# Kernel optimization log

Measured on AMD Instinct MI355X. Metric: run time of the kernel, lower is better.

## Reference

```python
import jax, jax.numpy as jnp
import numpy as np
from jax import lax

B, H, W, DIM = 64, 32, 32, 448
HEADS, DH, WS = 8, 28, 8
INNER = DH * HEADS            # 224
C2 = DIM // 2                 # 224 (spatial branch channels == inner_dim)
HALF = INNER // 2             # 112 per attention sub-branch
SEQ_L1 = WS * WS              # 64 tokens per window
SEQ_L2 = (256 // HEADS) ** 2 // SEQ_L1  # 16 == number of windows (32x32 map)
SCALE = DH ** -0.5


def setup_inputs() -> dict:
    key = jax.random.key(0)
    ks = jax.random.split(key, 18)
    def nrm(k, shape, s):
        return jax.random.normal(k, shape, jnp.float32) * s
    inp = {}
    inp["x"] = jax.random.normal(ks[0], (B, H, W, DIM), jnp.float32)
    # trunc_normal_(std=1) positional biases -> clipped normals
    inp["pos_emb1"] = jnp.clip(jax.random.normal(ks[1], (1, 1, HEADS // 2, SEQ_L1, SEQ_L1), jnp.float32), -2.0, 2.0)
    inp["pos_emb2"] = jnp.clip(jax.random.normal(ks[2], (1, 1, HEADS // 2, SEQ_L2, SEQ_L2), jnp.float32), -2.0, 2.0)
    # linear weights stored (in, out)
    inp["Wq"] = nrm(ks[3], (C2, INNER), 0.02)
    inp["Wkv"] = nrm(ks[4], (C2, 2 * INNER), 0.02)
    inp["Wout"] = nrm(ks[5], (INNER, DIM), 0.02)
    inp["bout"] = nrm(ks[6], (DIM,), 0.02)
    # 3D conv weights (O, I, D, Kh, Kw), fan-in = 224*27 -> std ~ 0.01
    for i, name in enumerate(["convr", "conv1", "conv2", "conv3"]):
        inp[name + "_w"] = nrm(ks[7 + 2 * i], (C2, C2, 3, 3, 3), 0.01)
        inp[name + "_b"] = nrm(ks[8 + 2 * i], (C2,), 0.01)
    return inp


def _conv3d(t, w, b):
    y = lax.conv_general_dilated(t, w, (1, 1, 1), [(1, 1)] * 3,
                                 dimension_numbers=("NCDHW", "OIDHW", "NCDHW"))
    return y + b[None, :, None, None, None]


def _window(t):
    # [b, H, W, c] -> [b, n_windows, ws*ws, c]
    b, h, w, c = t.shape
    t = t.reshape(b, h // WS, WS, w // WS, WS, c).transpose(0, 1, 3, 2, 4, 5)
    return t.reshape(b, (h // WS) * (w // WS), WS * WS, c)


def _unwindow(t):
    # [b, n_windows, ws*ws, c] -> [b, H, W, c]
    b, n, m, c = t.shape
    t = t.reshape(b, H // WS, W // WS, WS, WS, c).transpose(0, 1, 3, 2, 4, 5)
    return t.reshape(b, H, W, c)


def _split_heads(t):
    # [b, n, m, half] -> [b, n, heads//2, m, dh]
    b, n, m, c = t.shape
    return t.reshape(b, n, m, HEADS // 2, DH).transpose(0, 1, 3, 2, 4)


def _merge_heads(t):
    # [b, n, heads//2, m, dh] -> [b, n, m, half]
    b, n, h, m, d = t.shape
    return t.transpose(0, 1, 3, 2, 4).reshape(b, n, m, h * d)


def _attn(q, q_, k, v, pos):
    del q_
    sim = jnp.einsum("bnhid,bnhjd->bnhij", q * SCALE, k) + pos
    a = jax.nn.softmax(sim, axis=-1)
    return jnp.einsum("bnhij,bnhjd->bnhid", a, v)


def reference(x, pos_emb1, pos_emb2, Wq, Wkv, Wout, bout,
              convr_w, convr_b, conv1_w, conv1_b, conv2_w, conv2_b, conv3_w, conv3_b):
    b = x.shape[0]
    x1 = x[..., :C2]
    x2 = x[..., C2:]
    # spectral 3D conv branch: [b, c2, 1, H, W]
    x2 = x2.transpose(0, 3, 1, 2)[:, :, None]
    res = jax.nn.relu(_conv3d(x2, convr_w, convr_b))
    o = jax.nn.relu(_conv3d(x2, conv1_w, conv1_b))
    o = jax.nn.relu(_conv3d(o, conv2_w, conv2_b))
    o = jax.nn.relu(_conv3d(o, conv3_w, conv3_b))
    X2S = (o + res)[:, :, 0].transpose(0, 2, 3, 1)  # [b, H, W, c2]

    q = x1 @ Wq
    kv = x1 @ Wkv
    k, v = kv[..., :INNER], kv[..., INNER:]
    q1, q2 = q[..., :HALF], q[..., HALF:]
    k1, k2 = k[..., :HALF], k[..., HALF:]
    v1, v2 = v[..., :HALF], v[..., HALF:]

    # local (within-window) branch
    q1h, k1h, v1h = map(lambda t: _split_heads(_window(t)), (q1, k1, v1))
    sim1 = jnp.einsum("bnhid,bnhjd->bnhij", q1h * SCALE, k1h) + pos_emb1
    out1 = jnp.einsum("bnhij,bnhjd->bnhid", jax.nn.softmax(sim1, axis=-1), v1h)
    out1 = _merge_heads(out1)  # [b, n, m, half]

    # grid (across-window) branch: swap window/token axes
    q2h, k2h, v2h = map(lambda t: _split_heads(_window(t).transpose(0, 2, 1, 3)), (q2, k2, v2))
    sim2 = jnp.einsum("bnhid,bnhjd->bnhij", q2h * SCALE, k2h) + pos_emb2
    out2 = jnp.einsum("bnhij,bnhjd->bnhid", jax.nn.softmax(sim2, axis=-1), v2h)
    out2 = _merge_heads(out2).transpose(0, 2, 1, 3)  # [b, n, m, half]

    out = jnp.concatenate([out1, out2], axis=-1) @ Wout + bout  # [b, n, m, DIM]
    out = _unwindow(out)
    return jnp.concatenate([out, X2S], axis=-1)  # [b, H, W, DIM + C2]
```

## Files before the change

### kernel.cpp

```cpp
#include <hip/hip_runtime.h>

typedef unsigned short u16;
typedef unsigned int   u32;
typedef __attribute__((ext_vector_type(4))) float  f32x4;
typedef __attribute__((ext_vector_type(8))) short  s16x8;
typedef __attribute__((ext_vector_type(8))) __bf16 bf16x8;
typedef __attribute__((ext_vector_type(2))) u32    u32x2;

#define DEV __device__ __forceinline__
#define SCALE_Q 0.1889822365046136f

DEV float bf2f(u16 u){ u32 x = ((u32)u)<<16; float f; __builtin_memcpy(&f,&x,4); return f; }
DEV u16   f2bf(float f){ u32 x; __builtin_memcpy(&x,&f,4); return (u16)((x + 0x7fffu + ((x>>16)&1u))>>16); }

DEV s16x8 cvt8(const float* __restrict__ src){
  f32x4 f0 = *(const f32x4*)src, f1 = *(const f32x4*)(src+4);
  bf16x8 b;
  b[0]=(__bf16)f0[0]; b[1]=(__bf16)f0[1]; b[2]=(__bf16)f0[2]; b[3]=(__bf16)f0[3];
  b[4]=(__bf16)f1[0]; b[5]=(__bf16)f1[1]; b[6]=(__bf16)f1[2]; b[7]=(__bf16)f1[3];
  return __builtin_bit_cast(s16x8, b);
}

DEV void gll16(const u16* g, u16* l){
  __builtin_amdgcn_global_load_lds(
      (const __attribute__((address_space(1))) u32*)(const void*)g,
      (__attribute__((address_space(3))) u32*)(void*)l,
      16, 0, 0);
}

DEV void ld28(const u16* __restrict__ p, float* dst, float scale){
#pragma unroll
  for (int j=0;j<7;j++){
    u32x2 w = *(const u32x2*)(p + j*4);
    dst[j*4+0] = bf2f((u16)(w[0]&0xffffu))*scale;
    dst[j*4+1] = bf2f((u16)(w[0]>>16))*scale;
    dst[j*4+2] = bf2f((u16)(w[1]&0xffffu))*scale;
    dst[j*4+3] = bf2f((u16)(w[1]>>16))*scale;
  }
}

__global__ void pack_k(const float* __restrict__ Wq, const float* __restrict__ Wkv,
                       const float* __restrict__ Wout,
                       const float* __restrict__ wr, const float* __restrict__ w1,
                       const float* __restrict__ w2, const float* __restrict__ w3,
                       u16* __restrict__ WqkvT, u16* __restrict__ WoutT,
                       u16* __restrict__ convW)
{
  int idx = blockIdx.x*256 + threadIdx.x;
  if (idx < 150528) {
    int nn = idx/224, k = idx - nn*224;
    float v;
    if (nn < 224)      v = Wq [k*224 + nn];
    else if (nn < 448) v = Wkv[k*448 + (nn-224)];
    else               v = Wkv[k*448 + (nn-448) + 224];
    WqkvT[idx] = f2bf(v);
  } else if (idx < 250880) {
    int j = idx - 150528;
    int nn = j/224, k = j - nn*224;
    WoutT[j] = f2bf(Wout[k*448 + nn]);
  } else {
    int j = idx - 250880;
    int cv = j/451584, rem = j - cv*451584;
    int co = rem/2016, kk = rem - co*2016;
    int tap = kk/224, ci = kk - tap*224;
    const float* w = (cv==0)?wr:(cv==1)?w1:(cv==2)?w2:w3;
    convW[j] = f2bf(w[(co*224 + ci)*27 + 9 + tap]);
  }
}

__global__ void prep_k(const float* __restrict__ x, u16* __restrict__ x1bf,
                       u16* __restrict__ xpad, u16* __restrict__ oApad,
                       u16* __restrict__ oBpad)
{
  int idx = blockIdx.x*256 + threadIdx.x;
  int pp = idx/28, c8 = idx - pp*28;
  int b = pp/1156, rem = pp - b*1156, y = rem/34, xx = rem - y*34;
  int c0 = c8*8;
  if (y>=1 && y<=32 && xx>=1 && xx<=32){
    int p = (b*32 + y-1)*32 + (xx-1);
    *(s16x8*)(x1bf + p*224 + c0) = cvt8(x + p*448 + c0);
    *(s16x8*)(xpad + pp*224 + c0) = cvt8(x + p*448 + 224 + c0);
  } else {
    const s16x8 z = {0,0,0,0,0,0,0,0};
    *(s16x8*)(xpad  + pp*224 + c0) = z;
    *(s16x8*)(oApad + pp*224 + c0) = z;
    *(s16x8*)(oBpad + pp*224 + c0) = z;
  }
}

enum { M_FUSED=0, M_C2=1, M_C3=2, M_QKV=3, M_OUT=4 };

template<int MODE>
__global__ __launch_bounds__(512,4) void gemm_k(
    const u16* __restrict__ A, const u16* __restrict__ Bt,
    const float* __restrict__ bias0, const float* __restrict__ bias1,
    u16* __restrict__ outA, u16* __restrict__ outB, float* __restrict__ outF)
{
  constexpr bool CONV = (MODE==M_FUSED || MODE==M_C2 || MODE==M_C3);
  constexpr int KTOT = CONV ? 2016 : 224;
  constexpr int KS   = KTOT/32;

  __shared__ __align__(16) u16 Als[2][128*32];
  __shared__ __align__(16) u16 Bls[2][224*32];

  const int t  = threadIdx.x;
  const int bmRaw = blockIdx.x, nb = blockIdx.y;
  const int bm = ((bmRaw&7)<<6) + (bmRaw>>3);
  const int lane = t&63, lr = lane&15, lg = lane>>4;
  const int w = t>>6, wm = w>>1, wn = w&1;

  const int arow = t>>2;
  const int qsrc = ((t&3) - ((t>>4)&3)) & 3;
  const int acol8 = qsrc*8;
  const int p0 = bm*128 + arow;
  int PP0 = 0;
  if constexpr (CONV) PP0 = ((p0>>10)*34 + ((p0>>5)&31) + 1)*34 + (p0&31) + 1;
  const int Bb0 = (nb*224 +       arow)*KTOT + acol8;
  const int Bb1 = (nb*224 + 128 + arow)*KTOT + acol8;

  u16* aBase[2] = { &Als[0][0] + w*512, &Als[1][0] + w*512 };
  u16* bBase[2] = { &Bls[0][0] + w*512, &Bls[1][0] + w*512 };

  auto STAGE = [&](int buf, int ks){
    if constexpr (CONV){
      const int kc  = ks/9;
      const int tap = ks - kc*9;
      const int ty = tap/3, tx = tap - ty*3;
      const int toff = (ty-1)*34 + (tx-1);
      const int koff = tap*224 + kc*32;
      gll16(A + (PP0+toff)*224 + kc*32 + acol8, aBase[buf]);
      gll16(Bt + Bb0 + koff, bBase[buf]);
      if (w < 6) gll16(Bt + Bb1 + koff, bBase[buf] + 4096);
    } else {
      gll16(A + p0*224 + ks*32 + acol8, aBase[buf]);
      gll16(Bt + Bb0 + ks*32, bBase[buf]);
      if (w < 6) gll16(Bt + Bb1 + ks*32, bBase[buf] + 4096);
    }
  };

  f32x4 acc[2][7];
  { f32x4 zf = {0.f,0.f,0.f,0.f};
#pragma unroll
    for (int i=0;i<2;i++)
#pragma unroll
      for (int j=0;j<7;j++) acc[i][j] = zf; }

  STAGE(0, 0);
  __syncthreads();

  for (int ks=0; ks<KS; ++ks){
    const int cur = ks&1;
    if (ks+1 < KS) STAGE(cur^1, ks+1);

    const u16* Ac = &Als[cur][0];
    const u16* Bc = &Bls[cur][0];
    bf16x8 af[2], bfv[7];
#pragma unroll
    for (int mi=0; mi<2; ++mi){
      const int row = wm*32 + mi*16 + lr;
      af[mi] = *(const bf16x8*)(Ac + row*32 + ((lg + (row>>2))&3)*8);
    }
#pragma unroll
    for (int ni=0; ni<7; ++ni){
      const int row = wn*112 + ni*16 + lr;
      bfv[ni] = *(const bf16x8*)(Bc + row*32 + ((lg + (row>>2))&3)*8);
    }

#pragma unroll
    for (int ni=0; ni<7; ++ni)
#pragma unroll
      for (int mi=0; mi<2; ++mi)
        acc[mi][ni] = __builtin_amdgcn_mfma_f32_16x16x32_bf16(af[mi], bfv[ni], acc[mi][ni], 0,0,0);

    __syncthreads();
  }

  const float* bs;
  if constexpr (MODE==M_FUSED) bs = (nb==0) ? bias0 : bias1;
  else bs = bias0;

#pragma unroll
  for (int mi=0; mi<2; ++mi){
    const int rbase = bm*128 + wm*32 + mi*16 + lg*4;
#pragma unroll
    for (int ni=0; ni<7; ++ni){
      const int col = wn*112 + ni*16 + lr;
#pragma unroll
      for (int r=0;r<4;r++){
        const int row = rbase + r;
        float v = acc[mi][ni][r];
        if constexpr (MODE==M_FUSED){
          v = fmaxf(v + bs[col], 0.f);
          if (nb==0){
            outF[row*672 + 448 + col] = v;
          } else {
            const int pp = ((row>>10)*34 + ((row>>5)&31) + 1)*34 + (row&31) + 1;
            outB[pp*224 + col] = f2bf(v);
          }
        } else if constexpr (MODE==M_C2){
          v = fmaxf(v + bs[col], 0.f);
          const int pp = ((row>>10)*34 + ((row>>5)&31) + 1)*34 + (row&31) + 1;
          outB[pp*224 + col] = f2bf(v);
        } else if constexpr (MODE==M_C3){
          v = fmaxf(v + bs[col], 0.f);
          const int o = row*672 + 448 + col;
          outF[o] = v + outF[o];
        } else if constexpr (MODE==M_QKV){
          outA[row*672 + nb*224 + col] = f2bf(v);
        } else {
          outF[row*672 + nb*224 + col] = v + bs[nb*224 + col];
        }
      }
    }
  }
}

__global__ __launch_bounds__(256,2) void attn1_k(const u16* __restrict__ qkv,
    const float* __restrict__ pos1, u16* __restrict__ attnout)
{
  __shared__ __align__(16) float KL[64][112];
  __shared__ __align__(16) float VL[64][112];
  const int t = threadIdx.x;
  const int b = blockIdx.x>>4, n = blockIdx.x&15;
  const int base = b*1024 + (n>>2)*256 + (n&3)*8;
  {
    const int r = t>>2, part = t&3;
    const int pr_ = base + (r>>3)*32 + (r&7);
    const u16* kp = qkv + pr_*672 + 224 + part*28;
    const u16* vp = kp + 224;
#pragma unroll
    for (int j=0;j<7;j++){
      u32x2 kk = *(const u32x2*)(kp + j*4);
      u32x2 vv = *(const u32x2*)(vp + j*4);
      const int c = part*28 + j*4;
      KL[r][c+0]=bf2f((u16)(kk[0]&0xffffu)); KL[r][c+1]=bf2f((u16)(kk[0]>>16));
      KL[r][c+2]=bf2f((u16)(kk[1]&0xffffu)); KL[r][c+3]=bf2f((u16)(kk[1]>>16));
      VL[r][c+0]=bf2f((u16)(vv[0]&0xffffu)); VL[r][c+1]=bf2f((u16)(vv[0]>>16));
      VL[r][c+2]=bf2f((u16)(vv[1]&0xffffu)); VL[r][c+3]=bf2f((u16)(vv[1]>>16));
    }
  }
  __syncthreads();

  const int h = t>>6, i = t&63;
  const int pi = base + (i>>3)*32 + (i&7);
  float q[28];
  ld28(qkv + pi*672 + h*28, q, SCALE_Q);

  float s[64];
  const float* pr = pos1 + (h*64+i)*64;
#pragma unroll
  for (int j4=0;j4<16;j4++){
    f32x4 pv = *(const f32x4*)(pr + j4*4);
    s[j4*4+0]=pv[0]; s[j4*4+1]=pv[1]; s[j4*4+2]=pv[2]; s[j4*4+3]=pv[3];
  }
  const int c0 = h*28;
#pragma unroll
  for (int j=0;j<64;j++){
    const f32x4* kr = (const f32x4*)&KL[j][c0];
    float a0=0.f,a1=0.f,a2=0.f,a3=0.f;
#pragma unroll
    for (int u=0;u<7;u++){
      f32x4 kv = kr[u];
      a0 += q[u*4+0]*kv[0]; a1 += q[u*4+1]*kv[1];
      a2 += q[u*4+2]*kv[2]; a3 += q[u*4+3]*kv[3];
    }
    s[j] += (a0+a1)+(a2+a3);
  }
  float mx = s[0];
#pragma unroll
  for (int j=1;j<64;j++) mx = fmaxf(mx, s[j]);
  float sum = 0.f;
#pragma unroll
  for (int j=0;j<64;j++){ float e = __expf(s[j]-mx); s[j]=e; sum+=e; }
  const float inv = 1.f/sum;

  float out[28];
#pragma unroll
  for (int u=0;u<28;u++) out[u]=0.f;
#pragma unroll
  for (int j=0;j<64;j++){
    const float pj = s[j];
    const f32x4* vr = (const f32x4*)&VL[j][c0];
#pragma unroll
    for (int u=0;u<7;u++){
      f32x4 vv = vr[u];
      out[u*4+0] += pj*vv[0]; out[u*4+1] += pj*vv[1];
      out[u*4+2] += pj*vv[2]; out[u*4+3] += pj*vv[3];
    }
  }
  u16* op = attnout + pi*224 + h*28;
#pragma unroll
  for (int u=0;u<7;u++){
    u32x2 wv;
    wv[0] = (u32)f2bf(out[u*4+0]*inv) | ((u32)f2bf(out[u*4+1]*inv)<<16);
    wv[1] = (u32)f2bf(out[u*4+2]*inv) | ((u32)f2bf(out[u*4+3]*inv)<<16);
    *(u32x2*)(op + u*4) = wv;
  }
}

__global__ __launch_bounds__(256,1) void attn2_k(const u16* __restrict__ qkv,
    const float* __restrict__ pos2, u16* __restrict__ attnout)
{
  const int t = threadIdx.x;
  const int b = blockIdx.x>>4, mg = blockIdx.x&15;
  const int m = mg*4 + (t>>6);
  const int lane = t&63, h = lane>>4, i = lane&15;
  const int base = b*1024 + (m>>3)*32 + (m&7);
  const int pi = base + (i>>2)*256 + (i&3)*8;

  float q[28];
  ld28(qkv + pi*672 + 112 + h*28, q, SCALE_Q);

  float s[16];
  const float* pr = pos2 + (h*16+i)*16;
#pragma unroll
  for (int j4=0;j4<4;j4++){
    f32x4 pv = *(const f32x4*)(pr + j4*4);
    s[j4*4+0]=pv[0]; s[j4*4+1]=pv[1]; s[j4*4+2]=pv[2]; s[j4*4+3]=pv[3];
  }
#pragma unroll
  for (int j=0;j<16;j++){
    const int pj_ = base + (j>>2)*256 + (j&3)*8;
    float kk[28];
    ld28(qkv + pj_*672 + 336 + h*28, kk, 1.0f);
    float a=0.f;
#pragma unroll
    for (int u=0;u<28;u++) a += q[u]*kk[u];
    s[j] += a;
  }
  float mx = s[0];
#pragma unroll
  for (int j=1;j<16;j++) mx = fmaxf(mx, s[j]);
  float sum = 0.f;
#pragma unroll
  for (int j=0;j<16;j++){ float e = __expf(s[j]-mx); s[j]=e; sum+=e; }
  const float inv = 1.f/sum;

  float out[28];
#pragma unroll
  for (int u=0;u<28;u++) out[u]=0.f;
#pragma unroll
  for (int j=0;j<16;j++){
    const int pj_ = base + (j>>2)*256 + (j&3)*8;
    float vv[28];
    ld28(qkv + pj_*672 + 560 + h*28, vv, 1.0f);
    const float pj = s[j];
#pragma unroll
    for (int u=0;u<28;u++) out[u] += pj*vv[u];
  }
  u16* op = attnout + pi*224 + 112 + h*28;
#pragma unroll
  for (int u=0;u<7;u++){
    u32x2 wv;
    wv[0] = (u32)f2bf(out[u*4+0]*inv) | ((u32)f2bf(out[u*4+1]*inv)<<16);
    wv[1] = (u32)f2bf(out[u*4+2]*inv) | ((u32)f2bf(out[u*4+3]*inv)<<16);
    *(u32x2*)(op + u*4) = wv;
  }
}

extern "C" void kernel_launch(void* const* d_in, const int* in_sizes, int n_in,
                              void* d_out, int out_size, void* d_ws, size_t ws_size,
                              hipStream_t stream) {
  const float* x    = (const float*)d_in[0];
  const float* pos1 = (const float*)d_in[1];
  const float* pos2 = (const float*)d_in[2];
  const float* Wq   = (const float*)d_in[3];
  const float* Wkv  = (const float*)d_in[4];
  const float* Wout = (const float*)d_in[5];
  const float* bout = (const float*)d_in[6];
  const float* wr   = (const float*)d_in[7];
  const float* br   = (const float*)d_in[8];
  const float* w1   = (const float*)d_in[9];
  const float* b1   = (const float*)d_in[10];
  const float* w2   = (const float*)d_in[11];
  const float* b2   = (const float*)d_in[12];
  const float* w3   = (const float*)d_in[13];
  const float* b3   = (const float*)d_in[14];

  char* ws = (char*)d_ws;
  const size_t PADSZ = 73984ull*224*2;
  const size_t FLATS = 65536ull*224*2;
  u16* xpad   = (u16*)(ws);
  u16* oApad  = (u16*)(ws + PADSZ);
  u16* oBpad  = (u16*)(ws + 2*PADSZ);
  u16* x1bf   = (u16*)(ws + 3*PADSZ);
  u16* convW  = (u16*)(ws + 3*PADSZ + FLATS);
  u16* WqkvT  = convW + 4*451584;
  u16* WoutT  = WqkvT + 672*224;
  u16* qkv     = (u16*)(ws);
  u16* attnout = (u16*)(ws + 88080384);
  float* dout  = (float*)d_out;

  pack_k<<<8036, 256, 0, stream>>>(Wq, Wkv, Wout, wr, w1, w2, w3, WqkvT, WoutT, convW);
  prep_k<<<8092, 256, 0, stream>>>(x, x1bf, xpad, oApad, oBpad);

  gemm_k<M_FUSED><<<dim3(512,2), 512, 0, stream>>>(xpad,  convW,          br, b1, nullptr, oApad, dout);
  gemm_k<M_C2  ><<<dim3(512,1), 512, 0, stream>>>(oApad, convW+2*451584, b2, nullptr, nullptr, oBpad, nullptr);
  gemm_k<M_C3  ><<<dim3(512,1), 512, 0, stream>>>(oBpad, convW+3*451584, b3, nullptr, nullptr, nullptr, dout);

  gemm_k<M_QKV ><<<dim3(512,3), 512, 0, stream>>>(x1bf, WqkvT, nullptr, nullptr, qkv, nullptr, nullptr);
  attn1_k<<<1024, 256, 0, stream>>>(qkv, pos1, attnout);
  attn2_k<<<1024, 256, 0, stream>>>(qkv, pos2, attnout);
  gemm_k<M_OUT ><<<dim3(512,2), 512, 0, stream>>>(attnout, WoutT, bout, nullptr, nullptr, nullptr, dout);
}
```

Before: 510.6 us.

## Unroll conv K-loop over taps and merge the two attention kernels into one launch

The conv GEMM main loop is split into an outer channel-chunk loop and an inner tap loop unrolled by 9, so tap offsets become compile-time constants instead of per-iteration divisions. The A-fragment LDS addresses are hoisted out of the loop. The two attention kernels become device functions dispatched by block index inside one 2048-block kernel, which removes a launch and lets both branches run concurrently. The merged kernel always allocates attn1's LDS and uses launch bounds (256,2), which may limit occupancy or registers for the attn2 path that was previously compiled with (256,1).

```diff
diff --git a/kernel.cpp b/kernel.cpp
--- a/kernel.cpp
+++ b/kernel.cpp
@@ -121,21 +121,10 @@
   u16* aBase[2] = { &Als[0][0] + w*512, &Als[1][0] + w*512 };
   u16* bBase[2] = { &Bls[0][0] + w*512, &Bls[1][0] + w*512 };
 
-  auto STAGE = [&](int buf, int ks){
-    if constexpr (CONV){
-      const int kc  = ks/9;
-      const int tap = ks - kc*9;
-      const int ty = tap/3, tx = tap - ty*3;
-      const int toff = (ty-1)*34 + (tx-1);
-      const int koff = tap*224 + kc*32;
-      gll16(A + (PP0+toff)*224 + kc*32 + acol8, aBase[buf]);
-      gll16(Bt + Bb0 + koff, bBase[buf]);
-      if (w < 6) gll16(Bt + Bb1 + koff, bBase[buf] + 4096);
-    } else {
-      gll16(A + p0*224 + ks*32 + acol8, aBase[buf]);
-      gll16(Bt + Bb0 + ks*32, bBase[buf]);
-      if (w < 6) gll16(Bt + Bb1 + ks*32, bBase[buf] + 4096);
-    }
+  auto STAGE = [&](int buf, int aoff, int boff){
+    gll16(A + aoff, aBase[buf]);
+    gll16(Bt + Bb0 + boff, bBase[buf]);
+    if (w < 6) gll16(Bt + Bb1 + boff, bBase[buf] + 4096);
   };
 
   f32x4 acc[2][7];
@@ -145,34 +134,55 @@
 #pragma unroll
       for (int j=0;j<7;j++) acc[i][j] = zf; }
 
-  STAGE(0, 0);
-  __syncthreads();
-
-  for (int ks=0; ks<KS; ++ks){
-    const int cur = ks&1;
-    if (ks+1 < KS) STAGE(cur^1, ks+1);
-
+  const int rA0 = wm*32 + lr, rA1 = rA0 + 16;
+  const int cA0 = ((lg + (rA0>>2))&3)*8, cA1 = ((lg + (rA1>>2))&3)*8;
+
+  auto COMPUTE = [&](int cur){
     const u16* Ac = &Als[cur][0];
     const u16* Bc = &Bls[cur][0];
-    bf16x8 af[2], bfv[7];
-#pragma unroll
-    for (int mi=0; mi<2; ++mi){
-      const int row = wm*32 + mi*16 + lr;
-      af[mi] = *(const bf16x8*)(Ac + row*32 + ((lg + (row>>2))&3)*8);
-    }
+    bf16x8 af0 = *(const bf16x8*)(Ac + rA0*32 + cA0);
+    bf16x8 af1 = *(const bf16x8*)(Ac + rA1*32 + cA1);
+    bf16x8 bfv[7];
 #pragma unroll
     for (int ni=0; ni<7; ++ni){
       const int row = wn*112 + ni*16 + lr;
       bfv[ni] = *(const bf16x8*)(Bc + row*32 + ((lg + (row>>2))&3)*8);
     }
-
-#pragma unroll
-    for (int ni=0; ni<7; ++ni)
-#pragma unroll
-      for (int mi=0; mi<2; ++mi)
-        acc[mi][ni] = __builtin_amdgcn_mfma_f32_16x16x32_bf16(af[mi], bfv[ni], acc[mi][ni], 0,0,0);
-
+#pragma unroll
+    for (int ni=0; ni<7; ++ni){
+      acc[0][ni] = __builtin_amdgcn_mfma_f32_16x16x32_bf16(af0, bfv[ni], acc[0][ni], 0,0,0);
+      acc[1][ni] = __builtin_amdgcn_mfma_f32_16x16x32_bf16(af1, bfv[ni], acc[1][ni], 0,0,0);
+    }
+  };
+
+  if constexpr (CONV){
+    STAGE(0, (PP0-35)*224 + acol8, 0);
     __syncthreads();
+    int cur = 0;
+    for (int kc=0; kc<7; ++kc){
+#pragma unroll
+      for (int tap=0; tap<9; ++tap){
+        if (kc*9 + tap + 1 < KS){
+          const int tapn = (tap+1)%9;
+          const int kcn  = kc + (tap==8 ? 1:0);
+          const int tyn  = tapn/3, txn = tapn - tyn*3;
+          const int toffn = (tyn-1)*34 + (txn-1);
+          STAGE(cur^1, (PP0+toffn)*224 + kcn*32 + acol8, tapn*224 + kcn*32);
+        }
+        COMPUTE(cur);
+        __syncthreads();
+        cur ^= 1;
+      }
+    }
+  } else {
+    STAGE(0, p0*224 + acol8, 0);
+    __syncthreads();
+    for (int ks=0; ks<KS; ++ks){
+      const int cur = ks&1;
+      if (ks+1 < KS) STAGE(cur^1, p0*224 + (ks+1)*32 + acol8, (ks+1)*32);
+      COMPUTE(cur);
+      __syncthreads();
+    }
   }
 
   const float* bs;
@@ -215,13 +225,12 @@
   }
 }
 
-__global__ __launch_bounds__(256,2) void attn1_k(const u16* __restrict__ qkv,
-    const float* __restrict__ pos1, u16* __restrict__ attnout)
-{
-  __shared__ __align__(16) float KL[64][112];
-  __shared__ __align__(16) float VL[64][112];
+DEV void attn1_body(float (*KL)[112], float (*VL)[112],
+                    const u16* __restrict__ qkv, const float* __restrict__ pos1,
+                    u16* __restrict__ attnout, int blk)
+{
   const int t = threadIdx.x;
-  const int b = blockIdx.x>>4, n = blockIdx.x&15;
+  const int b = blk>>4, n = blk&15;
   const int base = b*1024 + (n>>2)*256 + (n&3)*8;
   {
     const int r = t>>2, part = t&3;
@@ -298,11 +307,11 @@
   }
 }
 
-__global__ __launch_bounds__(256,1) void attn2_k(const u16* __restrict__ qkv,
-    const float* __restrict__ pos2, u16* __restrict__ attnout)
+DEV void attn2_body(const u16* __restrict__ qkv, const float* __restrict__ pos2,
+                    u16* __restrict__ attnout, int blk)
 {
   const int t = threadIdx.x;
-  const int b = blockIdx.x>>4, mg = blockIdx.x&15;
+  const int b = blk>>4, mg = blk&15;
   const int m = mg*4 + (t>>6);
   const int lane = t&63, h = lane>>4, i = lane&15;
   const int base = b*1024 + (m>>3)*32 + (m&7);
@@ -356,6 +365,16 @@
     wv[1] = (u32)f2bf(out[u*4+2]*inv) | ((u32)f2bf(out[u*4+3]*inv)<<16);
     *(u32x2*)(op + u*4) = wv;
   }
+}
+
+__global__ __launch_bounds__(256,2) void attn12_k(const u16* __restrict__ qkv,
+    const float* __restrict__ pos1, const float* __restrict__ pos2,
+    u16* __restrict__ attnout)
+{
+  __shared__ __align__(16) float KL[64][112];
+  __shared__ __align__(16) float VL[64][112];
+  if (blockIdx.x < 1024) attn1_body(KL, VL, qkv, pos1, attnout, blockIdx.x);
+  else                   attn2_body(qkv, pos2, attnout, blockIdx.x - 1024);
 }
 
 extern "C" void kernel_launch(void* const* d_in, const int* in_sizes, int n_in,
@@ -399,7 +418,6 @@
   gemm_k<M_C3  ><<<dim3(512,1), 512, 0, stream>>>(oBpad, convW+3*451584, b3, nullptr, nullptr, nullptr, dout);
 
   gemm_k<M_QKV ><<<dim3(512,3), 512, 0, stream>>>(x1bf, WqkvT, nullptr, nullptr, qkv, nullptr, nullptr);
-  attn1_k<<<1024, 256, 0, stream>>>(qkv, pos1, attnout);
-  attn2_k<<<1024, 256, 0, stream>>>(qkv, pos2, attnout);
+  attn12_k<<<2048, 256, 0, stream>>>(qkv, pos1, pos2, attnout);
   gemm_k<M_OUT ><<<dim3(512,2), 512, 0, stream>>>(attnout, WoutT, bout, nullptr, nullptr, nullptr, dout);
 }
```

Result: no change. 509.0 us (-0.3%).
